# Performance work log

Hardware: AMD Instinct MI355X
Metric: run time of the kernel (lower is better)

Reference implementation:

```python
import jax, jax.numpy as jnp
import numpy as np
import math

S = 30.0
M = 0.5
COS_M = math.cos(M)
SIN_M = math.sin(M)
TH = math.cos(math.pi - M)  # threshold cos(pi - m)
EPS = 1e-12  # matches F.normalize default eps


def setup_inputs() -> dict:
    key = jax.random.key(0)
    k1, k2, k3 = jax.random.split(key, 3)
    B, D, C = 1024, 512, 100000
    inp = jax.random.normal(k1, (B, D), dtype=jnp.float32)
    label = jax.random.randint(k2, (B,), 0, C)
    # xavier_uniform_ for weight of shape (C, D): bound = sqrt(6/(C+D))
    bound = math.sqrt(6.0 / (C + D))
    weight = jax.random.uniform(k3, (C, D), dtype=jnp.float32, minval=-bound, maxval=bound)
    return {"input": inp, "label": label, "weight": weight}


def _l2norm(x):
    # F.normalize: x / max(||x||, eps)
    n = jnp.sqrt(jnp.sum(x * x, axis=-1, keepdims=True))
    return x / jnp.maximum(n, EPS)


def reference(input, label, weight):
    # cosine: [B, C]
    cosine = jnp.einsum('bd,cd->bc', _l2norm(input), _l2norm(weight))
    sine = jnp.sqrt(jnp.clip(1.0 - cosine * cosine, 0.0, 1.0))
    phi = cosine * COS_M - sine * SIN_M
    phi = jnp.where(cosine > TH, phi, cosine - S * SIN_M * M)
    # one-hot combine done via direct label-indexed select (avoids materializing one_hot)
    B, C = cosine.shape
    is_target = jnp.arange(C)[None, :] == label[:, None]  # [B, C] bool
    output = jnp.where(is_target, phi, cosine) * S
    return output
```

## Files before the change

kernel.cpp:

```cpp
#include <hip/hip_runtime.h>


#define MDIM 1024
#define KDIM 512
#define NCLS 100000

#define BM 128
#define BN 128
#define BK 32
#define LDST 40

#define NTILES ((NCLS + BN - 1) / BN)
#define NWG (8 * NTILES)

typedef unsigned short u16;
typedef unsigned int u32;
typedef short s16x8 __attribute__((ext_vector_type(8)));
typedef float f32x4 __attribute__((ext_vector_type(4)));

__device__ __forceinline__ u32 pk2(float a, float b) {
  u32 ua = __builtin_bit_cast(u32, a);
  u32 ub = __builtin_bit_cast(u32, b);
  ua += 0x7FFFu + ((ua >> 16) & 1u);
  ub += 0x7FFFu + ((ub >> 16) & 1u);
  return (ua >> 16) | (ub & 0xFFFF0000u);
}

__device__ __forceinline__ void gl16(const u16* g, u16* l) {
  __builtin_amdgcn_global_load_lds(
      (const __attribute__((address_space(1))) void*)g,
      (__attribute__((address_space(3))) void*)l, 16, 0, 0);
}

__global__ __launch_bounds__(256) void norm_input_kernel(const float* __restrict__ in,
                                                         u16* __restrict__ abf) {
  const int row = blockIdx.x;
  const int tid = threadIdx.x;
  const float2 v = *reinterpret_cast<const float2*>(in + (size_t)row * KDIM + 2 * tid);
  float ss = v.x * v.x + v.y * v.y;
#pragma unroll
  for (int off = 32; off > 0; off >>= 1) ss += __shfl_down(ss, off);
  __shared__ float part[4];
  if ((tid & 63) == 0) part[tid >> 6] = ss;
  __syncthreads();
  const float tot = part[0] + part[1] + part[2] + part[3];
  const float rn = 1.0f / fmaxf(sqrtf(tot), 1e-12f);
  reinterpret_cast<u32*>(abf)[row * (KDIM / 2) + tid] = pk2(v.x * rn, v.y * rn);
}

__global__ __launch_bounds__(256) void norm_weight_kernel(const float* __restrict__ W,
                                                          u16* __restrict__ wbf) {
  const int row = blockIdx.x * 4 + (threadIdx.x >> 6);
  const int lane = threadIdx.x & 63;
  const float* p = W + (size_t)row * KDIM + lane * 8;
  const float4 v0 = *reinterpret_cast<const float4*>(p);
  const float4 v1 = *reinterpret_cast<const float4*>(p + 4);
  float ss = v0.x * v0.x + v0.y * v0.y + v0.z * v0.z + v0.w * v0.w
           + v1.x * v1.x + v1.y * v1.y + v1.z * v1.z + v1.w * v1.w;
#pragma unroll
  for (int off = 32; off > 0; off >>= 1) ss += __shfl_xor(ss, off);
  const float rn = 1.0f / fmaxf(sqrtf(ss), 1e-12f);
  uint4 o;
  o.x = pk2(v0.x * rn, v0.y * rn);
  o.y = pk2(v0.z * rn, v0.w * rn);
  o.z = pk2(v1.x * rn, v1.y * rn);
  o.w = pk2(v1.z * rn, v1.w * rn);
  *reinterpret_cast<uint4*>(wbf + (size_t)row * KDIM + lane * 8) = o;
}

__global__ __launch_bounds__(256) void arcface_gemm_bf16(const u16* __restrict__ Abf,
                                                         const u16* __restrict__ Wbf,
                                                         const int* __restrict__ label,
                                                         float* __restrict__ out) {
  __shared__ u16 lA[BM * BK];
  __shared__ u16 lW[BN * BK];
  __shared__ int lbl[BM];

  const int tid = threadIdx.x;
  const int orig = blockIdx.x;
  const int wg = (orig & 7) * NTILES + (orig >> 3);
  const int m0 = (wg & 7) * BM;
  const int n0 = (wg >> 3) * BN;

  if (tid < BM) lbl[tid] = label[m0 + tid];

  const int lane = tid & 63;
  const int wv = tid >> 6;

  const int sr = lane & 15;
  const int sc = (lane >> 4) * 8;
  const u16* aG0 = Abf + (size_t)(m0 + 16 * wv + sr) * KDIM + sc;
  const u16* aG1 = aG0 + (size_t)64 * KDIM;
  int wr0 = n0 + 16 * wv + sr;       if (wr0 >= NCLS) wr0 = NCLS - 1;
  int wr1 = n0 + 64 + 16 * wv + sr;  if (wr1 >= NCLS) wr1 = NCLS - 1;
  const u16* wG0 = Wbf + (size_t)wr0 * KDIM + sc;
  const u16* wG1 = Wbf + (size_t)wr1 * KDIM + sc;
  u16* const lA0 = &lA[wv * 512];
  u16* const lA1 = &lA[(4 + wv) * 512];
  u16* const lW0 = &lW[wv * 512];
  u16* const lW1 = &lW[(4 + wv) * 512];

  f32x4 acc[4][4] = {};

  const int wm = (wv & 1) * 64;
  const int wn = (wv >> 1) * 64;
  const int ln = lane & 15;
  const int kq = lane >> 4;
  const int sA = wm >> 4;
  const int sW = wn >> 4;

  gl16(aG0, lA0); gl16(aG1, lA1); gl16(wG0, lW0); gl16(wG1, lW1);

  for (int kt = 0; kt < KDIM / BK; ++kt) {
    __syncthreads();

    s16x8 af[4], wf[4];
#pragma unroll
    for (int i = 0; i < 4; ++i)
      af[i] = *(const s16x8*)&lA[(sA + i) * 512 + kq * 128 + ln * 8];
#pragma unroll
    for (int j = 0; j < 4; ++j)
      wf[j] = *(const s16x8*)&lW[(sW + j) * 512 + kq * 128 + ln * 8];

    __syncthreads();

    if (kt < KDIM / BK - 1) {
      const int o = (kt + 1) * BK;
      gl16(aG0 + o, lA0); gl16(aG1 + o, lA1);
      gl16(wG0 + o, lW0); gl16(wG1 + o, lW1);
    }

#pragma unroll
    for (int i = 0; i < 4; ++i)
#pragma unroll
      for (int j = 0; j < 4; ++j)
        acc[i][j] = __builtin_amdgcn_mfma_f32_16x16x32_bf16(af[i], wf[j], acc[i][j], 0, 0, 0);
  }

  constexpr float S_ = 30.0f;
  constexpr float COS_M = 0.87758256189037276f;
  constexpr float SIN_M = 0.47942553860420301f;
  constexpr float TH_ = -0.87758256189037276f;
  constexpr float FALLB = 30.0f * 0.47942553860420301f * 0.5f;

#pragma unroll
  for (int i = 0; i < 4; ++i) {
    const int lrow_b = wm + 16 * i + 4 * kq;
#pragma unroll
    for (int j = 0; j < 4; ++j) {
      const int col = wn + 16 * j + ln;
      const int gcol = n0 + col;
      if (gcol < NCLS) {
#pragma unroll
        for (int rg = 0; rg < 4; ++rg) {
          const int lrow = lrow_b + rg;
          const float cosv = acc[i][j][rg];
          float o = S_ * cosv;
          if (gcol == lbl[lrow]) {
            const float s2 = fmaxf(1.0f - cosv * cosv, 0.0f);
            const float sine = sqrtf(s2);
            float phi = cosv * COS_M - sine * SIN_M;
            phi = (cosv > TH_) ? phi : (cosv - FALLB);
            o = S_ * phi;
          }
          out[(size_t)(m0 + lrow) * NCLS + gcol] = o;
        }
      }
    }
  }
}

__global__ __launch_bounds__(256) void arcface_gemm(const u16* __restrict__ Abf,
                                                    const float* __restrict__ W,
                                                    const int* __restrict__ label,
                                                    float* __restrict__ out) {
  __shared__ u16 lA[BM * LDST];
  __shared__ u16 lW[BN * LDST];
  __shared__ float rnw[BN];
  __shared__ int lbl[BM];

  const int tid = threadIdx.x;
  const int m0 = blockIdx.x * BM;
  const int n0 = blockIdx.y * BN;

  if (tid < BM) lbl[tid] = label[m0 + tid];

  const int r = tid >> 1;
  const int half = tid & 1;
  int c = n0 + r;
  if (c >= NCLS) c = NCLS - 1;

  const u16* aptr = Abf + (size_t)(m0 + r) * KDIM + half * 16;
  const float* wptr = W + (size_t)c * KDIM + half * 16;

  uint4 a0 = *(const uint4*)(aptr);
  uint4 a1 = *(const uint4*)(aptr + 8);
  float4 w0 = *(const float4*)(wptr);
  float4 w1 = *(const float4*)(wptr + 4);
  float4 w2 = *(const float4*)(wptr + 8);
  float4 w3 = *(const float4*)(wptr + 12);

  f32x4 acc[4][4] = {};
  float ss = 0.0f;

  const int lane = tid & 63;
  const int wv = tid >> 6;
  const int wm = (wv & 1) * 64;
  const int wn = (wv >> 1) * 64;
  const int ln = lane & 15;
  const int kq = lane >> 4;

  const int aw = r * LDST + half * 16;

  for (int kt = 0; kt < KDIM / BK; ++kt) {
    __syncthreads();
    *(uint4*)&lA[aw] = a0;
    *(uint4*)&lA[aw + 8] = a1;
    ss += w0.x * w0.x + w0.y * w0.y + w0.z * w0.z + w0.w * w0.w;
    ss += w1.x * w1.x + w1.y * w1.y + w1.z * w1.z + w1.w * w1.w;
    ss += w2.x * w2.x + w2.y * w2.y + w2.z * w2.z + w2.w * w2.w;
    ss += w3.x * w3.x + w3.y * w3.y + w3.z * w3.z + w3.w * w3.w;
    uint4 p0, p1;
    p0.x = pk2(w0.x, w0.y); p0.y = pk2(w0.z, w0.w);
    p0.z = pk2(w1.x, w1.y); p0.w = pk2(w1.z, w1.w);
    p1.x = pk2(w2.x, w2.y); p1.y = pk2(w2.z, w2.w);
    p1.z = pk2(w3.x, w3.y); p1.w = pk2(w3.z, w3.w);
    *(uint4*)&lW[aw] = p0;
    *(uint4*)&lW[aw + 8] = p1;
    __syncthreads();

    if (kt < KDIM / BK - 1) {
      const u16* ap = aptr + (kt + 1) * BK;
      a0 = *(const uint4*)(ap);
      a1 = *(const uint4*)(ap + 8);
      const float* wp = wptr + (kt + 1) * BK;
      w0 = *(const float4*)(wp);
      w1 = *(const float4*)(wp + 4);
      w2 = *(const float4*)(wp + 8);
      w3 = *(const float4*)(wp + 12);
    }

    s16x8 af[4], wf[4];
#pragma unroll
    for (int i = 0; i < 4; ++i)
      af[i] = *(const s16x8*)&lA[(wm + 16 * i + ln) * LDST + kq * 8];
#pragma unroll
    for (int j = 0; j < 4; ++j)
      wf[j] = *(const s16x8*)&lW[(wn + 16 * j + ln) * LDST + kq * 8];
#pragma unroll
    for (int i = 0; i < 4; ++i)
#pragma unroll
      for (int j = 0; j < 4; ++j)
        acc[i][j] = __builtin_amdgcn_mfma_f32_16x16x32_bf16(af[i], wf[j], acc[i][j], 0, 0, 0);
  }

  const float sst = ss + __shfl_xor(ss, 1);
  if (half == 0) rnw[r] = 1.0f / fmaxf(sqrtf(sst), 1e-12f);
  __syncthreads();

  constexpr float S_ = 30.0f;
  constexpr float COS_M = 0.87758256189037276f;
  constexpr float SIN_M = 0.47942553860420301f;
  constexpr float TH_ = -0.87758256189037276f;
  constexpr float FALLB = 30.0f * 0.47942553860420301f * 0.5f;

#pragma unroll
  for (int i = 0; i < 4; ++i) {
    const int lrow_b = wm + 16 * i + 4 * kq;
#pragma unroll
    for (int j = 0; j < 4; ++j) {
      const int col = wn + 16 * j + ln;
      const int gcol = n0 + col;
      const float rw = rnw[col];
      if (gcol < NCLS) {
#pragma unroll
        for (int rg = 0; rg < 4; ++rg) {
          const int lrow = lrow_b + rg;
          const float cosv = acc[i][j][rg] * rw;
          float o = S_ * cosv;
          if (gcol == lbl[lrow]) {
            const float s2 = fmaxf(1.0f - cosv * cosv, 0.0f);
            const float sine = sqrtf(s2);
            float phi = cosv * COS_M - sine * SIN_M;
            phi = (cosv > TH_) ? phi : (cosv - FALLB);
            o = S_ * phi;
          }
          out[(size_t)(m0 + lrow) * NCLS + gcol] = o;
        }
      }
    }
  }
}

extern "C" void kernel_launch(void* const* d_in, const int* in_sizes, int n_in,
                              void* d_out, int out_size, void* d_ws, size_t ws_size,
                              hipStream_t stream) {
  const float* input = (const float*)d_in[0];
  const int* label = (const int*)d_in[1];
  const float* weight = (const float*)d_in[2];
  float* out = (float*)d_out;
  u16* abf = (u16*)d_ws;

  hipLaunchKernelGGL(norm_input_kernel, dim3(MDIM), dim3(256), 0, stream, input, abf);

  const size_t a_bytes = (size_t)MDIM * KDIM * sizeof(u16);
  const size_t w_bytes = (size_t)NCLS * KDIM * sizeof(u16);
  if (ws_size >= a_bytes + w_bytes) {
    u16* wbf = abf + (size_t)MDIM * KDIM;
    hipLaunchKernelGGL(norm_weight_kernel, dim3(NCLS / 4), dim3(256), 0, stream, weight, wbf);
    hipLaunchKernelGGL(arcface_gemm_bf16, dim3(NWG), dim3(256), 0, stream, abf, wbf, label, out);
  } else {
    dim3 grid(MDIM / BM, (NCLS + BN - 1) / BN);
    hipLaunchKernelGGL(arcface_gemm, grid, dim3(256), 0, stream, abf, weight, label, out);
  }
}
```

Before: 785.1 us.

## Triple-buffer LDS tiles with two-stage-ahead prefetch and single barrier per k-step

Replaces the single LDS buffer and two syncthreads per k-step with three rotating LDS buffers. Global-to-LDS loads are issued two k-tiles ahead and waited on through explicit vmcnt counts, leaving one barrier per iteration. It also raises wave priority around the MFMA block and fully unrolls the k loop. The aim is to hide global-load latency behind compute. The cost is triple the LDS footprint, which may lower occupancy, and a dependence on the hand-written waitcnt values being correct.

Measured after the change: 781.6 us. No clear change (-0.4%).

```diff
diff --git a/kernel.cpp b/kernel.cpp
--- a/kernel.cpp
+++ b/kernel.cpp
@@ -72,8 +72,8 @@
                                                          const u16* __restrict__ Wbf,
                                                          const int* __restrict__ label,
                                                          float* __restrict__ out) {
-  __shared__ u16 lA[BM * BK];
-  __shared__ u16 lW[BN * BK];
+  __shared__ u16 lA[3][BM * BK];
+  __shared__ u16 lW[3][BN * BK];
   __shared__ int lbl[BM];
 
   const int tid = threadIdx.x;
@@ -95,10 +95,6 @@
   int wr1 = n0 + 64 + 16 * wv + sr;  if (wr1 >= NCLS) wr1 = NCLS - 1;
   const u16* wG0 = Wbf + (size_t)wr0 * KDIM + sc;
   const u16* wG1 = Wbf + (size_t)wr1 * KDIM + sc;
-  u16* const lA0 = &lA[wv * 512];
-  u16* const lA1 = &lA[(4 + wv) * 512];
-  u16* const lW0 = &lW[wv * 512];
-  u16* const lW1 = &lW[(4 + wv) * 512];
 
   f32x4 acc[4][4] = {};
 
@@ -109,33 +105,49 @@
   const int sA = wm >> 4;
   const int sW = wn >> 4;
 
-  gl16(aG0, lA0); gl16(aG1, lA1); gl16(wG0, lW0); gl16(wG1, lW1);
-
-  for (int kt = 0; kt < KDIM / BK; ++kt) {
-    __syncthreads();
-
+  constexpr int NT = KDIM / BK;
+
+#define STAGE(BUF, KT)                                   \
+  do {                                                   \
+    const int _o = (KT) * BK;                            \
+    gl16(aG0 + _o, &lA[(BUF)][wv * 512]);                \
+    gl16(aG1 + _o, &lA[(BUF)][(4 + wv) * 512]);          \
+    gl16(wG0 + _o, &lW[(BUF)][wv * 512]);                \
+    gl16(wG1 + _o, &lW[(BUF)][(4 + wv) * 512]);          \
+  } while (0)
+
+  STAGE(0, 0);
+  STAGE(1, 1);
+
+#pragma unroll
+  for (int kt = 0; kt < NT; ++kt) {
+    if (kt == NT - 1)
+      asm volatile("s_waitcnt vmcnt(0) lgkmcnt(0)" ::: "memory");
+    else
+      asm volatile("s_waitcnt vmcnt(4) lgkmcnt(0)" ::: "memory");
+    __builtin_amdgcn_s_barrier();
+    __builtin_amdgcn_sched_barrier(0);
+
+    const int b = kt % 3;
     s16x8 af[4], wf[4];
 #pragma unroll
     for (int i = 0; i < 4; ++i)
-      af[i] = *(const s16x8*)&lA[(sA + i) * 512 + kq * 128 + ln * 8];
+      af[i] = *(const s16x8*)&lA[b][(sA + i) * 512 + kq * 128 + ln * 8];
 #pragma unroll
     for (int j = 0; j < 4; ++j)
-      wf[j] = *(const s16x8*)&lW[(sW + j) * 512 + kq * 128 + ln * 8];
-
-    __syncthreads();
-
-    if (kt < KDIM / BK - 1) {
-      const int o = (kt + 1) * BK;
-      gl16(aG0 + o, lA0); gl16(aG1 + o, lA1);
-      gl16(wG0 + o, lW0); gl16(wG1 + o, lW1);
-    }
-
+      wf[j] = *(const s16x8*)&lW[b][(sW + j) * 512 + kq * 128 + ln * 8];
+
+    if (kt + 2 < NT) STAGE((kt + 2) % 3, kt + 2);
+
+    __builtin_amdgcn_s_setprio(1);
 #pragma unroll
     for (int i = 0; i < 4; ++i)
 #pragma unroll
       for (int j = 0; j < 4; ++j)
         acc[i][j] = __builtin_amdgcn_mfma_f32_16x16x32_bf16(af[i], wf[j], acc[i][j], 0, 0, 0);
-  }
+    __builtin_amdgcn_s_setprio(0);
+  }
+#undef STAGE
 
   constexpr float S_ = 30.0f;
   constexpr float COS_M = 0.87758256189037276f;
```
